# Performance work log

Measured on AMD Instinct MI355X. Metric: run time of the kernel, lower is better.

The kernel has to match this reference:

```python
import jax, jax.numpy as jnp
import numpy as np

EPS = 1e-5
CHUNK = 256
N_LAYERS = 4
D_MODEL = 1024
D_INNER = 2048
D_HEAD = 64
N_HEADS = 32
D_STATE = 64
D_CONV = 4
CONV_DIM = D_INNER + 2 * D_STATE  # ngroups=1
D_IN_PROJ = 2 * D_INNER + 2 * D_STATE + N_HEADS


def silu(x):
    return x * jax.nn.sigmoid(x)


def rmsnorm(x, w):
    return x * jax.lax.rsqrt(jnp.mean(x * x, axis=-1, keepdims=True) + EPS) * w


def segsum(x):
    # x: [..., T] -> [..., T, T] lower-triangular segment sums, -inf above diag
    T = x.shape[-1]
    cs = jnp.cumsum(x, axis=-1)
    ss = cs[..., :, None] - cs[..., None, :]
    mask = jnp.tril(jnp.ones((T, T), dtype=bool))
    return jnp.where(mask, ss, -jnp.inf)


def ssd(X, A, B, C, chunk):
    # X: [b,l,h,p] (already scaled by dt), A: [b,l,h] (= dt * A_head), B,C: [b,l,n] (ngroups=1)
    b, l, h, p = X.shape
    c = l // chunk
    X = X.reshape(b, c, chunk, h, p)
    A = A.reshape(b, c, chunk, h).transpose(0, 3, 1, 2)  # [b,h,c,l]
    B = B.reshape(b, c, chunk, -1)
    C = C.reshape(b, c, chunk, -1)
    Acs = jnp.cumsum(A, axis=-1)  # [b,h,c,l]
    # intra-chunk (diagonal blocks)
    Lm = jnp.exp(segsum(A))  # [b,h,c,l,l]
    Y_diag = jnp.einsum('bcln,bcsn,bhcls,bcshp->bclhp', C, B, Lm, X)
    # chunk end states
    decay_states = jnp.exp(Acs[..., -1:] - Acs)  # [b,h,c,l]
    states = jnp.einsum('bcln,bhcl,bclhp->bchpn', B, decay_states, X)
    # inter-chunk recurrence (c is small -> dense segsum over chunks)
    A_last = jnp.pad(Acs[..., -1], ((0, 0), (0, 0), (1, 0)))  # [b,h,c+1]
    decay_chunk = jnp.exp(segsum(A_last))  # [b,h,c+1,c+1]
    states = jnp.concatenate([jnp.zeros_like(states[:, :1]), states], axis=1)
    new_states = jnp.einsum('bhzc,bchpn->bzhpn', decay_chunk, states)
    states = new_states[:, :-1]  # state entering each chunk
    Y_off = jnp.einsum('bcln,bchpn,bhcl->bclhp', C, states, jnp.exp(Acs))
    return (Y_diag + Y_off).reshape(b, l, h, p)


def mamba2_layer(x, in_w, conv_w, conv_b, dt_bias, A_log, D, gnorm_w, out_w):
    b, l, _ = x.shape
    zxbcdt = jnp.einsum('bld,ed->ble', x, in_w)  # [b,l,D_IN_PROJ]
    z = zxbcdt[..., :D_INNER]
    xBC = zxbcdt[..., D_INNER:D_INNER + CONV_DIM]
    dt = zxbcdt[..., D_INNER + CONV_DIM:]  # [b,l,h]
    # depthwise causal conv1d + silu
    xpad = jnp.pad(xBC, ((0, 0), (D_CONV - 1, 0), (0, 0)))
    xconv = conv_b
    for k in range(D_CONV):
        xconv = xconv + xpad[:, k:k + l, :] * conv_w[:, k]
    xBC = silu(xconv)
    x_in = xBC[..., :D_INNER]
    B = xBC[..., D_INNER:D_INNER + D_STATE]
    C = xBC[..., D_INNER + D_STATE:]
    dt = jax.nn.softplus(dt + dt_bias)  # [b,l,h]
    A = -jnp.exp(A_log)  # [h]
    X = x_in.reshape(b, l, N_HEADS, D_HEAD)
    y = ssd(X * dt[..., None], dt * A, B, C, CHUNK)
    y = y + D[None, None, :, None] * X
    y = y.reshape(b, l, D_INNER)
    y = rmsnorm(y * silu(z), gnorm_w)
    return jnp.einsum('ble,de->bld', y, out_w)


def setup_inputs() -> dict:
    key = jax.random.key(0)
    ks = jax.random.split(key, 8)
    x = jax.random.normal(ks[0], (2, 2048, D_MODEL), dtype=jnp.float32)
    in_proj_w = jax.random.normal(ks[1], (N_LAYERS, D_IN_PROJ, D_MODEL), dtype=jnp.float32) * 0.02
    conv_w = jax.random.uniform(ks[2], (N_LAYERS, CONV_DIM, D_CONV), dtype=jnp.float32, minval=-0.5, maxval=0.5)
    conv_b = jnp.zeros((N_LAYERS, CONV_DIM), dtype=jnp.float32)
    A_log = jnp.log(jax.random.uniform(ks[3], (N_LAYERS, N_HEADS), dtype=jnp.float32, minval=1.0, maxval=16.0))
    dt0 = jax.random.uniform(ks[4], (N_LAYERS, N_HEADS), dtype=jnp.float32, minval=0.001, maxval=0.1)
    dt_bias = dt0 + jnp.log(-jnp.expm1(-dt0))  # inverse softplus
    D = jnp.ones((N_LAYERS, N_HEADS), dtype=jnp.float32)
    gnorm_w = jnp.ones((N_LAYERS, D_INNER), dtype=jnp.float32)
    out_proj_w = jax.random.normal(ks[5], (N_LAYERS, D_MODEL, D_INNER), dtype=jnp.float32) * 0.02
    rms_w = jnp.ones((N_LAYERS, D_MODEL), dtype=jnp.float32)
    return {"x": x, "in_proj_w": in_proj_w, "conv_w": conv_w, "conv_b": conv_b,
            "dt_bias": dt_bias, "A_log": A_log, "D": D, "gnorm_w": gnorm_w,
            "out_proj_w": out_proj_w, "rms_w": rms_w}


def reference(x, in_proj_w, conv_w, conv_b, dt_bias, A_log, D, gnorm_w, out_proj_w, rms_w):
    for i in range(N_LAYERS):
        x = x + mamba2_layer(rmsnorm(x, rms_w[i]), in_proj_w[i], conv_w[i], conv_b[i],
                             dt_bias[i], A_log[i], D[i], gnorm_w[i], out_proj_w[i])
    return x
```

## Files before the change

kernel.cpp:

```cpp
#include <hip/hip_runtime.h>
#include <cmath>

#define BATCH 2
#define LSEQ 2048
#define DMODEL 1024
#define DINNER 2048
#define NHEADS 32
#define DHEAD 64
#define DSTATE 64
#define DCONV 4
#define CONVDIM (DINNER + 2*DSTATE)
#define DINPROJ (2*DINNER + 2*DSTATE + NHEADS)
#define DINPROJ_PAD 4352
#define CHUNKSZ 256
#define NCHUNK (LSEQ/CHUNKSZ)
#define MROWS (BATCH*LSEQ)
#define EPSF 1e-5f

typedef __attribute__((ext_vector_type(8))) short shortx8;
typedef __attribute__((ext_vector_type(4))) short shortx4;
typedef __attribute__((ext_vector_type(4))) float floatx4;

__device__ __forceinline__ ushort f2bf(float f) {
  unsigned u = __float_as_uint(f);
  unsigned r = (u + 0x7fffu + ((u >> 16) & 1u)) >> 16;
  return (ushort)r;
}
__device__ __forceinline__ float bf2f(ushort b) {
  return __uint_as_float(((unsigned)b) << 16);
}

__device__ __forceinline__ shortx8 pack8(float4 a, float4 b) {
  shortx8 r;
  r[0] = (short)f2bf(a.x); r[1] = (short)f2bf(a.y);
  r[2] = (short)f2bf(a.z); r[3] = (short)f2bf(a.w);
  r[4] = (short)f2bf(b.x); r[5] = (short)f2bf(b.y);
  r[6] = (short)f2bf(b.z); r[7] = (short)f2bf(b.w);
  return r;
}

__device__ __forceinline__ void async_load16(const void* g, void* l) {
  __builtin_amdgcn_global_load_lds(
      (const __attribute__((address_space(1))) void*)g,
      (__attribute__((address_space(3))) void*)l, 16, 0, 0);
}

__device__ __forceinline__ float block_reduce_sum_256(float v, float* sb) {
  for (int off = 32; off > 0; off >>= 1) v += __shfl_down(v, off, 64);
  int lane = threadIdx.x & 63, wid = threadIdx.x >> 6;
  if (lane == 0) sb[wid] = v;
  __syncthreads();
  return sb[0] + sb[1] + sb[2] + sb[3];
}

__global__ __launch_bounds__(256) void cvt_bf16_k(const float* __restrict__ src,
                                                  ushort* __restrict__ dst,
                                                  size_t n_src, size_t n_dst) {
  size_t i = (size_t)blockIdx.x * 256 + threadIdx.x;
  if (i >= n_dst) return;
  float v = (i < n_src) ? src[i] : 0.f;
  dst[i] = f2bf(v);
}

__global__ __launch_bounds__(256) void cvt_w_all(const float* __restrict__ in_w,
                                                 const float* __restrict__ out_w,
                                                 ushort* __restrict__ in_bf,
                                                 ushort* __restrict__ out_bf) {
  unsigned g = (blockIdx.x * 256u + threadIdx.x) * 8u;
  const unsigned PL = (unsigned)DINPROJ_PAD * DMODEL;
  const unsigned n1 = 4u * PL;
  const unsigned n2 = 4u * DMODEL * DINNER;
  if (g < n1) {
    unsigned layer = g / PL, rem = g % PL;
    unsigned row = rem / DMODEL, col = rem % DMODEL;
    shortx8 o;
    if (row < DINPROJ) {
      const float* sp = in_w + ((size_t)layer * DINPROJ + row) * DMODEL + col;
      float4 a = *(const float4*)sp;
      float4 b = *(const float4*)(sp + 4);
      o = pack8(a, b);
    } else {
#pragma unroll
      for (int j = 0; j < 8; j++) o[j] = 0;
    }
    *(shortx8*)(in_bf + g) = o;
  } else if (g < n1 + n2) {
    unsigned j = g - n1;
    const float* sp = out_w + j;
    float4 a = *(const float4*)sp;
    float4 b = *(const float4*)(sp + 4);
    *(shortx8*)(out_bf + j) = pack8(a, b);
  }
}

__global__ __launch_bounds__(256) void rmsnorm_k(const float* __restrict__ x,
                                                 const float* __restrict__ w,
                                                 ushort* __restrict__ out) {
  __shared__ float sb[4];
  int r = blockIdx.x;
  const float* xr = x + (size_t)r * DMODEL;
  ushort* orow = out + (size_t)r * DMODEL;
  int c0 = threadIdx.x * 4;
  float4 v4 = *(const float4*)(xr + c0);
  float ssq = v4.x * v4.x + v4.y * v4.y + v4.z * v4.z + v4.w * v4.w;
  float s = block_reduce_sum_256(ssq, sb);
  float sc = rsqrtf(s / (float)DMODEL + EPSF);
  float4 w4 = *(const float4*)(w + c0);
  shortx4 o;
  o[0] = (short)f2bf(v4.x * sc * w4.x);
  o[1] = (short)f2bf(v4.y * sc * w4.y);
  o[2] = (short)f2bf(v4.z * sc * w4.z);
  o[3] = (short)f2bf(v4.w * sc * w4.w);
  *(shortx4*)(orow + c0) = o;
}

__device__ __forceinline__ void stage_tile(const ushort* __restrict__ A,
                                           const ushort* __restrict__ B,
                                           char* lb, int m0, int n0, int K, int k0,
                                           int wid, int rA, int sA) {
#pragma unroll
  for (int rd = 0; rd < 2; rd++) {
    int r = rd * 64 + rA;
    int sl = sA ^ ((r ^ (r >> 2)) & 3);
    async_load16(A + (size_t)(m0 + r) * K + (k0 + sl * 8), lb + rd * 4096 + wid * 1024);
  }
#pragma unroll
  for (int rd = 0; rd < 2; rd++) {
    int r = rd * 64 + rA;
    int sl = sA ^ ((r ^ (r >> 2)) & 3);
    async_load16(B + (size_t)(n0 + r) * K + (k0 + sl * 8), lb + 8192 + rd * 4096 + wid * 1024);
  }
}

template <int CFG>
__global__ __launch_bounds__(256, CFG == 0 ? 3 : 2) void gemm_nt_mfma_pipe(
    const ushort* __restrict__ A, const ushort* __restrict__ B,
    float* __restrict__ C, ushort* __restrict__ Cbf,
    const float* __restrict__ resid, int M, int N, int K,
    int nbx, int rw, int rh) {
  constexpr int NBUF = (CFG == 0) ? 3 : 5;
  __shared__ __align__(16) char lds[NBUF][16384];
  int tid = threadIdx.x;
  int wid = tid >> 6, lane = tid & 63;
  int quad = lane >> 4, lrow = lane & 15;

  int d = blockIdx.x;
  int xcd = d & 7, wi = d >> 3;
  int ra = nbx / rw;
  int rn = xcd % ra, rm = xcd / ra;
  int bx = rn * rw + wi % rw;
  int by = rm * rh + wi / rw;

  int m0 = by * 128, n0 = bx * 128;
  int wm = (wid >> 1) * 64, wn = (wid & 1) * 64;
  int rA = tid >> 2, sA = tid & 3;

  floatx4 acc[4][4];
#pragma unroll
  for (int i = 0; i < 4; i++)
#pragma unroll
    for (int j = 0; j < 4; j++) acc[i][j] = (floatx4){0.f, 0.f, 0.f, 0.f};

  int NT = K >> 5;
  constexpr int DEPTH = (CFG == 0) ? 2 : 3;
#pragma unroll
  for (int t = 0; t < DEPTH; t++)
    stage_tile(A, B, lds[t], m0, n0, K, t * 32, wid, rA, sA);

  int cur = 0, sb = DEPTH;
  for (int t = 0; t < NT; t++) {
    if (CFG == 1) {
      __builtin_amdgcn_sched_barrier(0);
      if (t + 3 < NT) {
        stage_tile(A, B, lds[sb], m0, n0, K, (t + 3) * 32, wid, rA, sA);
        sb = (sb == NBUF - 1) ? 0 : sb + 1;
      }
      int rem = NT - 1 - t;
      if (rem >= 3)      asm volatile("s_waitcnt vmcnt(12)" ::: "memory");
      else if (rem == 2) asm volatile("s_waitcnt vmcnt(8)" ::: "memory");
      else if (rem == 1) asm volatile("s_waitcnt vmcnt(4)" ::: "memory");
      else               asm volatile("s_waitcnt vmcnt(0)" ::: "memory");
      __builtin_amdgcn_s_barrier();
      __builtin_amdgcn_sched_barrier(0);
    } else {
      if (t < NT - 1) asm volatile("s_waitcnt vmcnt(4)" ::: "memory");
      else            asm volatile("s_waitcnt vmcnt(0)" ::: "memory");
      __builtin_amdgcn_s_barrier();
      __builtin_amdgcn_sched_barrier(0);
      if (t + 2 < NT) {
        stage_tile(A, B, lds[sb], m0, n0, K, (t + 2) * 32, wid, rA, sA);
        sb = (sb == NBUF - 1) ? 0 : sb + 1;
      }
    }

    const char* Ab = lds[cur];
    const char* Bb = Ab + 8192;
    cur = (cur == NBUF - 1) ? 0 : cur + 1;
    shortx8 af[4], bfr[4];
#pragma unroll
    for (int i = 0; i < 4; i++) {
      int r = wm + i * 16 + lrow;
      af[i] = *(const shortx8*)(Ab + r * 64 + ((quad ^ ((r ^ (r >> 2)) & 3)) << 4));
    }
#pragma unroll
    for (int j = 0; j < 4; j++) {
      int r = wn + j * 16 + lrow;
      bfr[j] = *(const shortx8*)(Bb + r * 64 + ((quad ^ ((r ^ (r >> 2)) & 3)) << 4));
    }
    __builtin_amdgcn_s_setprio(1);
#pragma unroll
    for (int i = 0; i < 4; i++)
#pragma unroll
      for (int j = 0; j < 4; j++)
        acc[i][j] = __builtin_amdgcn_mfma_f32_16x16x32_bf16(af[i], bfr[j], acc[i][j], 0, 0, 0);
    __builtin_amdgcn_s_setprio(0);
  }

  if (Cbf) {
#pragma unroll
    for (int i = 0; i < 4; i++) {
      int r0 = m0 + wm + i * 16 + quad * 4;
#pragma unroll
      for (int j = 0; j < 4; j++) {
        int n = n0 + wn + j * 16 + lrow;
        if (n < N)
#pragma unroll
          for (int r = 0; r < 4; r++)
            Cbf[(size_t)(r0 + r) * N + n] = f2bf(acc[i][j][r]);
      }
    }
  } else {
    bool hasR = (resid != nullptr);
#pragma unroll
    for (int i = 0; i < 4; i++) {
      int r0 = m0 + wm + i * 16 + quad * 4;
#pragma unroll
      for (int j = 0; j < 4; j++) {
        int n = n0 + wn + j * 16 + lrow;
        if (n < N) {
#pragma unroll
          for (int r = 0; r < 4; r++) {
            size_t idx = (size_t)(r0 + r) * N + n;
            float v = acc[i][j][r];
            if (hasR) v += resid[idx];
            C[idx] = v;
          }
        }
      }
    }
  }
}

__global__ __launch_bounds__(256) void convcum_k(const ushort* __restrict__ zxbf,
                                                 const float* __restrict__ cw,
                                                 const float* __restrict__ cb,
                                                 ushort* __restrict__ xbf,
                                                 const float* __restrict__ dt_bias,
                                                 const float* __restrict__ A_log,
                                                 float* __restrict__ dt_sp,
                                                 float* __restrict__ dtA_cs) {
  __shared__ float buf[256];
  int tid = threadIdx.x;
  if (blockIdx.x < MROWS / 8) {
    int r0 = blockIdx.x * 8;
    int bstart = r0 & ~(LSEQ - 1);
#pragma unroll
    for (int rep = 0; rep < 2; rep++) {
      int ch;
      if (rep == 0) ch = tid * 8;
      else { if (tid >= (CONVDIM - 2048) / 8) break; ch = 2048 + tid * 8; }
      float wv[8][4], bias[8];
#pragma unroll
      for (int j = 0; j < 8; j++) {
        float4 w4 = *(const float4*)(cw + (ch + j) * 4);
        wv[j][0] = w4.x; wv[j][1] = w4.y; wv[j][2] = w4.z; wv[j][3] = w4.w;
        bias[j] = cb[ch + j];
      }
      float xw[11][8];
#pragma unroll
      for (int wr = 0; wr < 11; wr++) {
        int rr = r0 - 3 + wr;
        if (rr < bstart) {
#pragma unroll
          for (int j = 0; j < 8; j++) xw[wr][j] = 0.f;
        } else {
          shortx8 v = *(const shortx8*)(zxbf + (size_t)rr * DINPROJ + DINNER + ch);
#pragma unroll
          for (int j = 0; j < 8; j++) xw[wr][j] = bf2f((ushort)v[j]);
        }
      }
#pragma unroll
      for (int o = 0; o < 8; o++) {
        shortx8 ov;
#pragma unroll
        for (int j = 0; j < 8; j++) {
          float acc = bias[j];
#pragma unroll
          for (int k = 0; k < 4; k++) acc += xw[o + k][j] * wv[j][k];
          float s = acc / (1.f + expf(-acc));
          ov[j] = (short)f2bf(s);
        }
        *(shortx8*)(xbf + (size_t)(r0 + o) * CONVDIM + ch) = ov;
      }
    }
  } else {
    int bid = blockIdx.x - MROWS / 8;
    int h = bid & 31, c = (bid >> 5) & 7, b = bid >> 8;
    int l = tid;
    float Aneg = -expf(A_log[h]);
    int row = b * LSEQ + c * CHUNKSZ + l;
    float v = bf2f(zxbf[(size_t)row * DINPROJ + DINNER + CONVDIM + h]) + dt_bias[h];
    float dtv = (v > 20.f) ? v : log1pf(expf(v));
    dt_sp[row * 32 + h] = dtv;
    buf[l] = dtv * Aneg;
    __syncthreads();
    for (int off = 1; off < 256; off <<= 1) {
      float add = (l >= off) ? buf[l - off] : 0.f;
      __syncthreads();
      buf[l] += add;
      __syncthreads();
    }
    dtA_cs[(size_t)bid * CHUNKSZ + l] = buf[l];
  }
}

#define ST_STRIDE 72
__global__ __launch_bounds__(256) void states_mfma(const ushort* __restrict__ xbf,
                                                   const float* __restrict__ dt_sp,
                                                   const float* __restrict__ dtA_cs,
                                                   float* __restrict__ st_raw) {
  __shared__ ushort XT[64 * ST_STRIDE];
  __shared__ ushort BT[64 * ST_STRIDE];
  __shared__ float wrow[64];
  int bid = blockIdx.x;
  int h = bid & 31, c = (bid >> 5) & 7, b = bid >> 8;
  int tid = threadIdx.x;
  int w = tid >> 6, lane = tid & 63;
  int quad = lane >> 4, lrow = lane & 15;
  int cbase = bid * CHUNKSZ;
  int rowbase = b * LSEQ + c * CHUNKSZ;
  float T = dtA_cs[cbase + CHUNKSZ - 1];
  floatx4 acc[4];
  for (int jt = 0; jt < 4; jt++) acc[jt] = (floatx4){0.f, 0.f, 0.f, 0.f};
  int half = tid & 31, srb = tid >> 5;
  int ekey = (half & 7) << 3;
  for (int lt = 0; lt < 4; lt++) {
    __syncthreads();
    if (tid < 64) {
      int row = rowbase + lt * 64 + tid;
      wrow[tid] = dt_sp[row * 32 + h] * __expf(T - dtA_cs[cbase + lt * 64 + tid]);
    }
    __syncthreads();
    for (int pass = 0; pass < 8; pass++) {
      int sr = srb + pass * 8;
      int row = rowbase + lt * 64 + sr;
      uint bv = *(const uint*)(xbf + (size_t)row * CONVDIM + DINNER + 2 * half);
      uint xv = *(const uint*)(xbf + (size_t)row * CONVDIM + h * DHEAD + 2 * half);
      float wv = wrow[sr];
      int sc = sr ^ ekey;
      BT[(2 * half) * ST_STRIDE + sc]     = (ushort)(bv & 0xffff);
      BT[(2 * half + 1) * ST_STRIDE + sc] = (ushort)(bv >> 16);
      XT[(2 * half) * ST_STRIDE + sc]     = f2bf(bf2f((ushort)(xv & 0xffff)) * wv);
      XT[(2 * half + 1) * ST_STRIDE + sc] = f2bf(bf2f((ushort)(xv >> 16)) * wv);
    }
    __syncthreads();
    int arow = w * 16 + lrow;
    int akey = ((arow >> 1) & 7) << 3;
    for (int kk = 0; kk < 64; kk += 32) {
      shortx8 af = *(const shortx8*)&XT[arow * ST_STRIDE + ((kk + quad * 8) ^ akey)];
      for (int jt = 0; jt < 4; jt++) {
        int brow = jt * 16 + lrow;
        int bkey = ((brow >> 1) & 7) << 3;
        shortx8 bf = *(const shortx8*)&BT[brow * ST_STRIDE + ((kk + quad * 8) ^ bkey)];
        acc[jt] = __builtin_amdgcn_mfma_f32_16x16x32_bf16(af, bf, acc[jt], 0, 0, 0);
      }
    }
  }
  size_t base = (size_t)bid * (DHEAD * DSTATE);
  for (int jt = 0; jt < 4; jt++) {
    int n = jt * 16 + lrow;
    for (int r = 0; r < 4; r++) {
      int p = w * 16 + quad * 4 + r;
      st_raw[base + (size_t)p * 64 + n] = acc[jt][r];
    }
  }
}

__global__ __launch_bounds__(256) void scan_k(float* __restrict__ st,
                                              const float* __restrict__ dtA_cs) {
  int bid = blockIdx.x;
  int seg = bid & 3, h = (bid >> 2) & 31, b = bid >> 7;
  int tid = threadIdx.x;
  int off = seg * 1024;
  float s[4];
  for (int i = 0; i < 4; i++) s[i] = 0.f;
  for (int c = 0; c < NCHUNK; c++) {
    int g = (b * NCHUNK + c) * 32 + h;
    float dec = expf(dtA_cs[(size_t)g * CHUNKSZ + CHUNKSZ - 1]);
    size_t base = (size_t)g * (DHEAD * DSTATE) + off;
    for (int i = 0; i < 4; i++) {
      int idx = tid + i * 256;
      float raw = st[base + idx];
      st[base + idx] = s[i];
      s[i] = s[i] * dec + raw;
    }
  }
}

#define BS_STRIDE 72
#define XT_STRIDE 68
#define PW_STRIDE 72
__global__ __launch_bounds__(256) void ydiag_mfma(const ushort* __restrict__ xbf,
                                                  const float* __restrict__ dt_sp,
                                                  const float* __restrict__ dtA_cs,
                                                  const float* __restrict__ st_in,
                                                  ushort* __restrict__ Y) {
  __shared__ ushort Bs[64 * BS_STRIDE];
  __shared__ ushort XsT[64 * XT_STRIDE];
  __shared__ ushort Pw[4 * 16 * PW_STRIDE];
  __shared__ float cs[256];
  int tid = threadIdx.x;
  int w = tid >> 6, lane = tid & 63;
  int quad = lane >> 4, lrow = lane & 15;
  int bid = blockIdx.x;
  int lt = bid & 3, h = (bid >> 2) & 31, c = (bid >> 7) & 7, b = bid >> 10;
  int g = (b * NCHUNK + c) * 32 + h;
  int cbase = g * CHUNKSZ;
  int rowbase = b * LSEQ + c * CHUNKSZ;

  cs[tid] = dtA_cs[cbase + tid];
  __syncthreads();

  int mrow = lt * 64 + w * 16;
  float csl[4];
  for (int r = 0; r < 4; r++) csl[r] = cs[mrow + quad * 4 + r];

  shortx8 Cf[2];
  {
    const ushort* cp = xbf + (size_t)(rowbase + mrow + lrow) * CONVDIM + DINNER + DSTATE;
    for (int q = 0; q < 2; q++)
      Cf[q] = *(const shortx8*)(cp + q * 32 + quad * 8);
  }

  floatx4 acc[4];
  for (int jt = 0; jt < 4; jt++) acc[jt] = (floatx4){0.f, 0.f, 0.f, 0.f};
  const float* stp = st_in + (size_t)g * (DHEAD * DSTATE);
  for (int q = 0; q < 2; q++) {
    for (int jt = 0; jt < 4; jt++) {
      const float* sp = stp + (size_t)(jt * 16 + lrow) * 64 + q * 32 + quad * 8;
      shortx8 sf = pack8(*(const float4*)sp, *(const float4*)(sp + 4));
      acc[jt] = __builtin_amdgcn_mfma_f32_16x16x32_bf16(Cf[q], sf, acc[jt], 0, 0, 0);
    }
  }
  for (int jt = 0; jt < 4; jt++)
    for (int r = 0; r < 4; r++) acc[jt][r] *= __expf(csl[r]);

  ushort* myP = Pw + w * 16 * PW_STRIDE;
  int half = tid & 31, srb = tid >> 5;
  for (int st = 0; st <= lt; st++) {
    __syncthreads();
    for (int pass = 0; pass < 8; pass++) {
      int sr = srb + pass * 8;
      int row = rowbase + st * 64 + sr;
      uint bv = *(const uint*)(xbf + (size_t)row * CONVDIM + DINNER + 2 * half);
      *(uint*)&Bs[sr * BS_STRIDE + 2 * half] = bv;
      float dtv = dt_sp[row * 32 + h];
      uint xv = *(const uint*)(xbf + (size_t)row * CONVDIM + h * DHEAD + 2 * half);
      XsT[(2 * half) * XT_STRIDE + sr]     = f2bf(bf2f((ushort)(xv & 0xffff)) * dtv);
      XsT[(2 * half + 1) * XT_STRIDE + sr] = f2bf(bf2f((ushort)(xv >> 16)) * dtv);
    }
    __syncthreads();
    for (int jt = 0; jt < 4; jt++) {
      floatx4 s = (floatx4){0.f, 0.f, 0.f, 0.f};
      for (int q = 0; q < 2; q++) {
        shortx8 bfr = *(const shortx8*)&Bs[(jt * 16 + lrow) * BS_STRIDE + q * 32 + quad * 8];
        s = __builtin_amdgcn_mfma_f32_16x16x32_bf16(Cf[q], bfr, s, 0, 0, 0);
      }
      int scol = st * 64 + jt * 16 + lrow;
      float css = cs[scol];
      for (int r = 0; r < 4; r++) {
        int l = mrow + quad * 4 + r;
        float v = (scol <= l) ? s[r] * __expf(csl[r] - css) : 0.f;
        myP[(quad * 4 + r) * PW_STRIDE + jt * 16 + lrow] = f2bf(v);
      }
    }
    shortx8 pf[2];
    for (int q = 0; q < 2; q++)
      pf[q] = *(const shortx8*)&myP[lrow * PW_STRIDE + q * 32 + quad * 8];
    for (int jt = 0; jt < 4; jt++) {
      for (int q = 0; q < 2; q++) {
        const ushort* xp = &XsT[(jt * 16 + lrow) * XT_STRIDE + q * 32 + quad * 8];
        shortx4 lo = *(const shortx4*)xp;
        shortx4 hi = *(const shortx4*)(xp + 4);
        shortx8 xf = __builtin_shufflevector(lo, hi, 0, 1, 2, 3, 4, 5, 6, 7);
        acc[jt] = __builtin_amdgcn_mfma_f32_16x16x32_bf16(pf[q], xf, acc[jt], 0, 0, 0);
      }
    }
  }
  int growb = rowbase + mrow + quad * 4;
  for (int jt = 0; jt < 4; jt++)
    for (int r = 0; r < 4; r++)
      Y[(size_t)(growb + r) * DINNER + h * DHEAD + jt * 16 + lrow] = f2bf(acc[jt][r]);
}

__global__ __launch_bounds__(256) void gatenorm_k(const ushort* __restrict__ Ybf,
                                                  const ushort* __restrict__ zxbf,
                                                  const ushort* __restrict__ xbf,
                                                  const float* __restrict__ Dvec,
                                                  const float* __restrict__ gw,
                                                  ushort* __restrict__ obf) {
  __shared__ float sb[4];
  int r = blockIdx.x;
  int c0 = threadIdx.x * 8;
  const ushort* yr = Ybf + (size_t)r * DINNER;
  const ushort* zr = zxbf + (size_t)r * DINPROJ;
  const ushort* xr = xbf + (size_t)r * CONVDIM;
  ushort* orow = obf + (size_t)r * DINNER;
  shortx8 y8 = *(const shortx8*)(yr + c0);
  shortx8 z8 = *(const shortx8*)(zr + c0);
  shortx8 x8 = *(const shortx8*)(xr + c0);
  float Dv = Dvec[threadIdx.x >> 3];
  float t[8]; float ssq = 0.f;
#pragma unroll
  for (int i = 0; i < 8; i++) {
    float z = bf2f((ushort)z8[i]);
    float yv = bf2f((ushort)y8[i]) + Dv * bf2f((ushort)x8[i]);
    float gv = yv * (z / (1.f + expf(-z)));
    t[i] = gv;
    ssq += gv * gv;
  }
  float s = block_reduce_sum_256(ssq, sb);
  float sc = rsqrtf(s / (float)DINNER + EPSF);
  float4 g0 = *(const float4*)(gw + c0);
  float4 g1 = *(const float4*)(gw + c0 + 4);
  shortx8 o;
  o[0] = (short)f2bf(t[0] * sc * g0.x); o[1] = (short)f2bf(t[1] * sc * g0.y);
  o[2] = (short)f2bf(t[2] * sc * g0.z); o[3] = (short)f2bf(t[3] * sc * g0.w);
  o[4] = (short)f2bf(t[4] * sc * g1.x); o[5] = (short)f2bf(t[5] * sc * g1.y);
  o[6] = (short)f2bf(t[6] * sc * g1.z); o[7] = (short)f2bf(t[7] * sc * g1.w);
  *(shortx8*)(orow + c0) = o;
}

extern "C" void kernel_launch(void* const* d_in, const int* in_sizes, int n_in,
                              void* d_out, int out_size, void* d_ws, size_t ws_size,
                              hipStream_t stream) {
  const float* x_in     = (const float*)d_in[0];
  const float* in_w     = (const float*)d_in[1];
  const float* conv_w   = (const float*)d_in[2];
  const float* conv_b   = (const float*)d_in[3];
  const float* dt_bias  = (const float*)d_in[4];
  const float* A_log    = (const float*)d_in[5];
  const float* Dvec     = (const float*)d_in[6];
  const float* gnorm_w  = (const float*)d_in[7];
  const float* out_w    = (const float*)d_in[8];
  const float* rms_w    = (const float*)d_in[9];
  float* out = (float*)d_out;

  float* ws = (float*)d_ws;
  size_t o = 0;
  float* x_cur  = ws + o; o += (size_t)MROWS * DMODEL;
  ushort* zx_bf = (ushort*)(ws + o); o += (size_t)MROWS * DINPROJ / 2;
  ushort* xbf   = (ushort*)(ws + o); o += (size_t)MROWS * CONVDIM / 2;
  float* dt_sp  = ws + o; o += (size_t)MROWS * NHEADS;
  float* dtA_cs = ws + o; o += (size_t)BATCH * NCHUNK * NHEADS * CHUNKSZ;
  float* st     = ws + o; o += (size_t)BATCH * NCHUNK * NHEADS * DHEAD * DSTATE;
  ushort* Ybf   = (ushort*)(ws + o); o += (size_t)MROWS * DINNER / 2;
  ushort* act_bf = (ushort*)(ws + o); o += (size_t)MROWS * DINNER / 2;
  size_t base_f = o;

  size_t inw_f  = (size_t)4 * DINPROJ_PAD * DMODEL / 2;
  size_t outw_f = (size_t)4 * DMODEL * DINNER / 2;
  bool hoist = ws_size >= (base_f + inw_f + outw_f) * sizeof(float);

  ushort* in_bf_all = (ushort*)(ws + base_f);
  ushort* out_bf_all = (ushort*)(ws + base_f + inw_f);
  ushort* w_bf_fb = (ushort*)(ws + base_f);

  hipMemcpyAsync(x_cur, x_in, (size_t)MROWS * DMODEL * sizeof(float),
                 hipMemcpyDeviceToDevice, stream);

  if (hoist) {
    unsigned ntot = (4u * DINPROJ_PAD * DMODEL + 4u * DMODEL * DINNER) / 8u;
    cvt_w_all<<<(ntot + 255) / 256, 256, 0, stream>>>(in_w, out_w, in_bf_all, out_bf_all);
  }

  for (int i = 0; i < 4; i++) {
    const float* conv_w_i = conv_w  + (size_t)i * CONVDIM * DCONV;
    const float* conv_b_i = conv_b  + (size_t)i * CONVDIM;
    const float* dtb_i    = dt_bias + (size_t)i * NHEADS;
    const float* Alog_i   = A_log   + (size_t)i * NHEADS;
    const float* D_i      = Dvec    + (size_t)i * NHEADS;
    const float* gw_i     = gnorm_w + (size_t)i * DINNER;
    const float* rms_w_i  = rms_w   + (size_t)i * DMODEL;

    const ushort* w1_bf;
    const ushort* w2_bf;
    if (hoist) {
      w1_bf = in_bf_all  + (size_t)i * DINPROJ_PAD * DMODEL;
      w2_bf = out_bf_all + (size_t)i * DMODEL * DINNER;
    } else {
      size_t ns = (size_t)DINPROJ * DMODEL, nd = (size_t)DINPROJ_PAD * DMODEL;
      cvt_bf16_k<<<(nd + 255) / 256, 256, 0, stream>>>(
          in_w + (size_t)i * DINPROJ * DMODEL, w_bf_fb, ns, nd);
      w1_bf = w_bf_fb;
      w2_bf = w_bf_fb;
    }

    rmsnorm_k<<<MROWS, 256, 0, stream>>>(x_cur, rms_w_i, act_bf);
    gemm_nt_mfma_pipe<0><<<(DINPROJ_PAD / 128) * (MROWS / 128), 256, 0, stream>>>(
        act_bf, w1_bf, nullptr, zx_bf, nullptr, MROWS, DINPROJ, DMODEL,
        DINPROJ_PAD / 128, 17, 8);
    convcum_k<<<MROWS / 8 + BATCH * NCHUNK * NHEADS, 256, 0, stream>>>(
        zx_bf, conv_w_i, conv_b_i, xbf, dtb_i, Alog_i, dt_sp, dtA_cs);
    states_mfma<<<BATCH * NCHUNK * NHEADS, 256, 0, stream>>>(xbf, dt_sp, dtA_cs, st);
    scan_k<<<BATCH * NHEADS * 4, 256, 0, stream>>>(st, dtA_cs);
    ydiag_mfma<<<BATCH * NCHUNK * NHEADS * 4, 256, 0, stream>>>(
        xbf, dt_sp, dtA_cs, st, Ybf);
    gatenorm_k<<<MROWS, 256, 0, stream>>>(Ybf, zx_bf, xbf, D_i, gw_i, act_bf);
    if (!hoist) {
      size_t ns = (size_t)DMODEL * DINNER;
      cvt_bf16_k<<<(ns + 255) / 256, 256, 0, stream>>>(
          out_w + (size_t)i * DMODEL * DINNER, (ushort*)w_bf_fb, ns, ns);
    }
    float* outC = (i == 3) ? out : x_cur;
    gemm_nt_mfma_pipe<1><<<(DMODEL / 128) * (MROWS / 128), 256, 0, stream>>>(
        act_bf, w2_bf, outC, nullptr, x_cur, MROWS, DMODEL, DINNER,
        DMODEL / 128, 4, 8);
  }
}
```

Measured before the change: 911.9 us.

## Use 128x64 tiles with shallower pipeline for out-projection GEMM

Replaces the out-projection GEMM (M=4096, N=1024, K=2048) with a dedicated kernel using 128x64 output tiles, which doubles the block count from 256 to 512 for better CU occupancy on a 256-CU device. It also drops the 5-buffer, depth-3 prefetch pipeline in favor of a 3-buffer, depth-2 pipeline. The in-projection GEMM loses its template parameter but keeps the same behavior. The trade-off is less B-tile reuse per block and more redundant loading of A tiles.

```diff
diff --git a/kernel.cpp b/kernel.cpp
--- a/kernel.cpp
+++ b/kernel.cpp
@@ -132,14 +132,11 @@
   }
 }
 
-template <int CFG>
-__global__ __launch_bounds__(256, CFG == 0 ? 3 : 2) void gemm_nt_mfma_pipe(
+__global__ __launch_bounds__(256, 3) void gemm_nt_mfma_pipe(
     const ushort* __restrict__ A, const ushort* __restrict__ B,
-    float* __restrict__ C, ushort* __restrict__ Cbf,
-    const float* __restrict__ resid, int M, int N, int K,
+    ushort* __restrict__ Cbf, int M, int N, int K,
     int nbx, int rw, int rh) {
-  constexpr int NBUF = (CFG == 0) ? 3 : 5;
-  __shared__ __align__(16) char lds[NBUF][16384];
+  __shared__ __align__(16) char lds[3][16384];
   int tid = threadIdx.x;
   int wid = tid >> 6, lane = tid & 63;
   int quad = lane >> 4, lrow = lane & 15;
@@ -162,40 +159,24 @@
     for (int j = 0; j < 4; j++) acc[i][j] = (floatx4){0.f, 0.f, 0.f, 0.f};
 
   int NT = K >> 5;
-  constexpr int DEPTH = (CFG == 0) ? 2 : 3;
-#pragma unroll
-  for (int t = 0; t < DEPTH; t++)
+#pragma unroll
+  for (int t = 0; t < 2; t++)
     stage_tile(A, B, lds[t], m0, n0, K, t * 32, wid, rA, sA);
 
-  int cur = 0, sb = DEPTH;
+  int cur = 0, sb = 2;
   for (int t = 0; t < NT; t++) {
-    if (CFG == 1) {
-      __builtin_amdgcn_sched_barrier(0);
-      if (t + 3 < NT) {
-        stage_tile(A, B, lds[sb], m0, n0, K, (t + 3) * 32, wid, rA, sA);
-        sb = (sb == NBUF - 1) ? 0 : sb + 1;
-      }
-      int rem = NT - 1 - t;
-      if (rem >= 3)      asm volatile("s_waitcnt vmcnt(12)" ::: "memory");
-      else if (rem == 2) asm volatile("s_waitcnt vmcnt(8)" ::: "memory");
-      else if (rem == 1) asm volatile("s_waitcnt vmcnt(4)" ::: "memory");
-      else               asm volatile("s_waitcnt vmcnt(0)" ::: "memory");
-      __builtin_amdgcn_s_barrier();
-      __builtin_amdgcn_sched_barrier(0);
-    } else {
-      if (t < NT - 1) asm volatile("s_waitcnt vmcnt(4)" ::: "memory");
-      else            asm volatile("s_waitcnt vmcnt(0)" ::: "memory");
-      __builtin_amdgcn_s_barrier();
-      __builtin_amdgcn_sched_barrier(0);
-      if (t + 2 < NT) {
-        stage_tile(A, B, lds[sb], m0, n0, K, (t + 2) * 32, wid, rA, sA);
-        sb = (sb == NBUF - 1) ? 0 : sb + 1;
-      }
+    if (t < NT - 1) asm volatile("s_waitcnt vmcnt(4)" ::: "memory");
+    else            asm volatile("s_waitcnt vmcnt(0)" ::: "memory");
+    __builtin_amdgcn_s_barrier();
+    __builtin_amdgcn_sched_barrier(0);
+    if (t + 2 < NT) {
+      stage_tile(A, B, lds[sb], m0, n0, K, (t + 2) * 32, wid, rA, sA);
+      sb = (sb == 2) ? 0 : sb + 1;
     }
 
     const char* Ab = lds[cur];
     const char* Bb = Ab + 8192;
-    cur = (cur == NBUF - 1) ? 0 : cur + 1;
+    cur = (cur == 2) ? 0 : cur + 1;
     shortx8 af[4], bfr[4];
 #pragma unroll
     for (int i = 0; i < 4; i++) {
@@ -216,36 +197,115 @@
     __builtin_amdgcn_s_setprio(0);
   }
 
-  if (Cbf) {
+#pragma unroll
+  for (int i = 0; i < 4; i++) {
+    int r0 = m0 + wm + i * 16 + quad * 4;
+#pragma unroll
+    for (int j = 0; j < 4; j++) {
+      int n = n0 + wn + j * 16 + lrow;
+      if (n < N)
+#pragma unroll
+        for (int r = 0; r < 4; r++)
+          Cbf[(size_t)(r0 + r) * N + n] = f2bf(acc[i][j][r]);
+    }
+  }
+}
+
+__device__ __forceinline__ void stage_tile64(const ushort* __restrict__ A,
+                                             const ushort* __restrict__ B,
+                                             char* lb, int m0, int n0, int K, int k0,
+                                             int wid, int rA, int sA) {
+#pragma unroll
+  for (int rd = 0; rd < 2; rd++) {
+    int r = rd * 64 + rA;
+    int sl = sA ^ ((r ^ (r >> 2)) & 3);
+    async_load16(A + (size_t)(m0 + r) * K + (k0 + sl * 8), lb + rd * 4096 + wid * 1024);
+  }
+  {
+    int r = rA;
+    int sl = sA ^ ((r ^ (r >> 2)) & 3);
+    async_load16(B + (size_t)(n0 + r) * K + (k0 + sl * 8), lb + 8192 + wid * 1024);
+  }
+}
+
+__global__ __launch_bounds__(256, 2) void gemm_nt_64(
+    const ushort* __restrict__ A, const ushort* __restrict__ B,
+    float* __restrict__ C, const float* __restrict__ resid,
+    int M, int N, int K, int nbx, int rw, int rh) {
+  __shared__ __align__(16) char lds[3][12288];
+  int tid = threadIdx.x;
+  int wid = tid >> 6, lane = tid & 63;
+  int quad = lane >> 4, lrow = lane & 15;
+
+  int d = blockIdx.x;
+  int xcd = d & 7, wi = d >> 3;
+  int ra = nbx / rw;
+  int rn = xcd % ra, rm = xcd / ra;
+  int bx = rn * rw + wi % rw;
+  int by = rm * rh + wi / rw;
+
+  int m0 = by * 128, n0 = bx * 64;
+  int wm = (wid >> 1) * 64, wn = (wid & 1) * 32;
+  int rA = tid >> 2, sA = tid & 3;
+
+  floatx4 acc[4][2];
+#pragma unroll
+  for (int i = 0; i < 4; i++)
+#pragma unroll
+    for (int j = 0; j < 2; j++) acc[i][j] = (floatx4){0.f, 0.f, 0.f, 0.f};
+
+  int NT = K >> 5;
+#pragma unroll
+  for (int t = 0; t < 2; t++)
+    stage_tile64(A, B, lds[t], m0, n0, K, t * 32, wid, rA, sA);
+
+  int cur = 0, sb = 2;
+  for (int t = 0; t < NT; t++) {
+    if (t < NT - 1) asm volatile("s_waitcnt vmcnt(3)" ::: "memory");
+    else            asm volatile("s_waitcnt vmcnt(0)" ::: "memory");
+    __builtin_amdgcn_s_barrier();
+    __builtin_amdgcn_sched_barrier(0);
+    if (t + 2 < NT) {
+      stage_tile64(A, B, lds[sb], m0, n0, K, (t + 2) * 32, wid, rA, sA);
+      sb = (sb == 2) ? 0 : sb + 1;
+    }
+
+    const char* Ab = lds[cur];
+    const char* Bb = Ab + 8192;
+    cur = (cur == 2) ? 0 : cur + 1;
+    shortx8 af[4], bfr[2];
 #pragma unroll
     for (int i = 0; i < 4; i++) {
-      int r0 = m0 + wm + i * 16 + quad * 4;
-#pragma unroll
-      for (int j = 0; j < 4; j++) {
-        int n = n0 + wn + j * 16 + lrow;
-        if (n < N)
-#pragma unroll
-          for (int r = 0; r < 4; r++)
-            Cbf[(size_t)(r0 + r) * N + n] = f2bf(acc[i][j][r]);
-      }
-    }
-  } else {
-    bool hasR = (resid != nullptr);
-#pragma unroll
-    for (int i = 0; i < 4; i++) {
-      int r0 = m0 + wm + i * 16 + quad * 4;
-#pragma unroll
-      for (int j = 0; j < 4; j++) {
-        int n = n0 + wn + j * 16 + lrow;
-        if (n < N) {
-#pragma unroll
-          for (int r = 0; r < 4; r++) {
-            size_t idx = (size_t)(r0 + r) * N + n;
-            float v = acc[i][j][r];
-            if (hasR) v += resid[idx];
-            C[idx] = v;
-          }
-        }
+      int r = wm + i * 16 + lrow;
+      af[i] = *(const shortx8*)(Ab + r * 64 + ((quad ^ ((r ^ (r >> 2)) & 3)) << 4));
+    }
+#pragma unroll
+    for (int j = 0; j < 2; j++) {
+      int r = wn + j * 16 + lrow;
+      bfr[j] = *(const shortx8*)(Bb + r * 64 + ((quad ^ ((r ^ (r >> 2)) & 3)) << 4));
+    }
+    __builtin_amdgcn_s_setprio(1);
+#pragma unroll
+    for (int i = 0; i < 4; i++)
+#pragma unroll
+      for (int j = 0; j < 2; j++)
+        acc[i][j] = __builtin_amdgcn_mfma_f32_16x16x32_bf16(af[i], bfr[j], acc[i][j], 0, 0, 0);
+    __builtin_amdgcn_s_setprio(0);
+  }
+
+  bool hasR = (resid != nullptr);
+#pragma unroll
+  for (int i = 0; i < 4; i++) {
+    int r0 = m0 + wm + i * 16 + quad * 4;
+#pragma unroll
+    for (int j = 0; j < 2; j++) {
+      int n = n0 + wn + j * 16 + lrow;
+#pragma unroll
+      for (int r = 0; r < 4; r++) {
+        size_t idx = (size_t)(r0 + r) * N + n;
+        float v = acc[i][j][r];
+        if (hasR) v += resid[idx];
+        C[idx] = v;
       }
     }
   }
@@ -607,9 +667,8 @@
     }
 
     rmsnorm_k<<<MROWS, 256, 0, stream>>>(x_cur, rms_w_i, act_bf);
-    gemm_nt_mfma_pipe<0><<<(DINPROJ_PAD / 128) * (MROWS / 128), 256, 0, stream>>>(
-        act_bf, w1_bf, nullptr, zx_bf, nullptr, MROWS, DINPROJ, DMODEL,
-        DINPROJ_PAD / 128, 17, 8);
+    gemm_nt_mfma_pipe<<<(DINPROJ_PAD / 128) * (MROWS / 128), 256, 0, stream>>>(
+        act_bf, w1_bf, zx_bf, MROWS, DINPROJ, DMODEL, DINPROJ_PAD / 128, 17, 8);
     convcum_k<<<MROWS / 8 + BATCH * NCHUNK * NHEADS, 256, 0, stream>>>(
         zx_bf, conv_w_i, conv_b_i, xbf, dtb_i, Alog_i, dt_sp, dtA_cs);
     states_mfma<<<BATCH * NCHUNK * NHEADS, 256, 0, stream>>>(xbf, dt_sp, dtA_cs, st);
@@ -623,8 +682,7 @@
           out_w + (size_t)i * DMODEL * DINNER, (ushort*)w_bf_fb, ns, ns);
     }
     float* outC = (i == 3) ? out : x_cur;
-    gemm_nt_mfma_pipe<1><<<(DMODEL / 128) * (MROWS / 128), 256, 0, stream>>>(
-        act_bf, w2_bf, outC, nullptr, x_cur, MROWS, DMODEL, DINNER,
-        DMODEL / 128, 4, 8);
-  }
-}
+    gemm_nt_64<<<(MROWS / 128) * (DMODEL / 64), 256, 0, stream>>>(
+        act_bf, w2_bf, outC, x_cur, MROWS, DMODEL, DINNER, DMODEL / 64, 8, 8);
+  }
+}
```

Result: faster. 887.4 us (-2.7%).
